# Kernel tuning notes

Measured on AMD Instinct MI355X. Metric: run time of the kernel, lower is better.

The kernel has to match this reference:

```python
import jax, jax.numpy as jnp
import numpy as np

N = 50000          # nodes
E_RAND = 800000    # random edges (avg degree 16)
IN, HID, HEADS, OUT = 256, 64, 4, 40
NEG_SLOPE = 0.2    # PyG GATConv default leaky_relu slope
BN_EPS = 1e-5


def setup_inputs() -> dict:
    key = jax.random.key(0)
    ks = jax.random.split(key, 24)
    x = jax.random.normal(ks[0], (N, IN), jnp.float32)
    ei = jax.random.randint(ks[1], (2, E_RAND), 0, N)
    loops = jnp.arange(N, dtype=ei.dtype)
    edge_index = jnp.concatenate([ei, jnp.stack([loops, loops])], axis=1)  # add self loops (PyG default)
    s = 0.1
    d = {
        "x": x,
        "edge_index": edge_index,
        "W0": jax.random.normal(ks[2], (IN, HEADS * HID), jnp.float32) * s,
        "a_src0": jax.random.normal(ks[3], (HEADS, HID), jnp.float32) * s,
        "a_dst0": jax.random.normal(ks[4], (HEADS, HID), jnp.float32) * s,
        "b0": jax.random.normal(ks[5], (HEADS * HID,), jnp.float32) * s,
        "bn0_g": jnp.ones((HEADS * HID,), jnp.float32),
        "bn0_b": jnp.zeros((HEADS * HID,), jnp.float32),
        "bn0_m": jax.random.normal(ks[6], (HEADS * HID,), jnp.float32) * s,
        "bn0_v": jax.random.uniform(ks[7], (HEADS * HID,), jnp.float32, 0.5, 1.5),
        "W1": jax.random.normal(ks[8], (HEADS * HID, HEADS * HID), jnp.float32) * s,
        "a_src1": jax.random.normal(ks[9], (HEADS, HID), jnp.float32) * s,
        "a_dst1": jax.random.normal(ks[10], (HEADS, HID), jnp.float32) * s,
        "b1": jax.random.normal(ks[11], (HEADS * HID,), jnp.float32) * s,
        "bn1_g": jnp.ones((HEADS * HID,), jnp.float32),
        "bn1_b": jnp.zeros((HEADS * HID,), jnp.float32),
        "bn1_m": jax.random.normal(ks[12], (HEADS * HID,), jnp.float32) * s,
        "bn1_v": jax.random.uniform(ks[13], (HEADS * HID,), jnp.float32, 0.5, 1.5),
        "W2": jax.random.normal(ks[14], (HEADS * HID, OUT), jnp.float32) * s,
        "a_src2": jax.random.normal(ks[15], (1, OUT), jnp.float32) * s,
        "a_dst2": jax.random.normal(ks[16], (1, OUT), jnp.float32) * s,
        "b2": jax.random.normal(ks[17], (OUT,), jnp.float32) * s,
    }
    return d


def gat_conv(x, edge_index, W, att_src, att_dst, heads, ch):
    """PyG GATConv (eval mode): gather -> leaky_relu attn -> segment softmax -> scatter add."""
    src, dst = edge_index[0], edge_index[1]
    h = (x @ W).reshape(-1, heads, ch)                       # [N,H,C]
    a_s = jnp.einsum('nhc,hc->nh', h, att_src)
    a_d = jnp.einsum('nhc,hc->nh', h, att_dst)
    e = jax.nn.leaky_relu(a_s[src] + a_d[dst], NEG_SLOPE)    # [E,H]
    m = jax.ops.segment_max(e, dst, num_segments=N)
    m = jax.lax.stop_gradient(jnp.where(jnp.isfinite(m), m, 0.0))
    p = jnp.exp(e - m[dst])
    denom = jax.ops.segment_sum(p, dst, num_segments=N)
    alpha = p / (denom[dst] + 1e-16)                         # [E,H]
    msg = h[src] * alpha[:, :, None]                         # [E,H,C]
    return jax.ops.segment_sum(msg, dst, num_segments=N)     # [N,H,C]


def _bn(h, g, b, m, v):
    return g * (h - m) * jax.lax.rsqrt(v + BN_EPS) + b


def reference(x, edge_index, W0, a_src0, a_dst0, b0, bn0_g, bn0_b, bn0_m, bn0_v,
              W1, a_src1, a_dst1, b1, bn1_g, bn1_b, bn1_m, bn1_v,
              W2, a_src2, a_dst2, b2):
    h = gat_conv(x, edge_index, W0, a_src0, a_dst0, HEADS, HID).reshape(N, HEADS * HID) + b0
    h = jax.nn.elu(_bn(h, bn0_g, bn0_b, bn0_m, bn0_v))
    h = gat_conv(h, edge_index, W1, a_src1, a_dst1, HEADS, HID).reshape(N, HEADS * HID) + b1
    h = jax.nn.elu(_bn(h, bn1_g, bn1_b, bn1_m, bn1_v))
    out = gat_conv(h, edge_index, W2, a_src2, a_dst2, 1, OUT).reshape(N, OUT) + b2
    return out
```

## Files before the change

### kernel.cpp

```cpp
#include <hip/hip_runtime.h>
#include <cstdint>
#include <cstddef>

constexpr int kN = 50000;
constexpr float kSlope = 0.2f;
constexpr float kBnEps = 1e-5f;

static inline int ceil_div(int a, int b) { return (a + b - 1) / b; }

typedef __attribute__((ext_vector_type(8))) short bf16x8;
typedef __attribute__((ext_vector_type(8))) unsigned short ushortx8;
typedef __attribute__((ext_vector_type(4))) float f32x4;

__device__ inline unsigned short f2bf(float f) {
  unsigned int u = __float_as_uint(f);
  u = (u + 0x7FFFu + ((u >> 16) & 1u)) >> 16;
  return (unsigned short)u;
}
__device__ inline float bf2f(unsigned short h) {
  return __uint_as_float(((unsigned int)h) << 16);
}


__global__ void k_degree(const int* __restrict__ dst, int* __restrict__ deg, int E) {
  int e = blockIdx.x * blockDim.x + threadIdx.x;
  if (e < E) atomicAdd(&deg[dst[e]], 1);
}

__global__ void k_scan1(const int* __restrict__ deg, int* __restrict__ rp,
                        int* __restrict__ bsum, int n) {
  __shared__ int sm[256];
  int i = blockIdx.x * 256 + threadIdx.x;
  int v = (i < n) ? deg[i] : 0;
  sm[threadIdx.x] = v;
  __syncthreads();
  for (int off = 1; off < 256; off <<= 1) {
    int t = (threadIdx.x >= off) ? sm[threadIdx.x - off] : 0;
    __syncthreads();
    sm[threadIdx.x] += t;
    __syncthreads();
  }
  if (i < n) rp[i + 1] = sm[threadIdx.x];
  if (threadIdx.x == 255) bsum[blockIdx.x] = sm[255];
}

__global__ void k_scan2(int* bsum, int nb) {
  __shared__ int sm[256];
  int v = (threadIdx.x < nb) ? bsum[threadIdx.x] : 0;
  sm[threadIdx.x] = v;
  __syncthreads();
  for (int off = 1; off < 256; off <<= 1) {
    int t = (threadIdx.x >= off) ? sm[threadIdx.x - off] : 0;
    __syncthreads();
    sm[threadIdx.x] += t;
    __syncthreads();
  }
  if (threadIdx.x < nb) bsum[threadIdx.x] = sm[threadIdx.x] - v;
}

__global__ void k_scan3(int* __restrict__ rp, const int* __restrict__ bsum, int n) {
  int i = blockIdx.x * 256 + threadIdx.x;
  if (i < n) rp[i + 1] += bsum[blockIdx.x];
  if (i == 0) rp[0] = 0;
}

__global__ void k_scatter(const int* __restrict__ src, const int* __restrict__ dst,
                          const int* __restrict__ rp, int* __restrict__ cur,
                          int* __restrict__ csr, int E) {
  int e = blockIdx.x * blockDim.x + threadIdx.x;
  if (e < E) {
    int d = dst[e];
    int pos = rp[d] + atomicAdd(&cur[d], 1);
    csr[pos] = src[e];
  }
}


__global__ void k_cast(const float* __restrict__ in, unsigned short* __restrict__ out, int n4) {
  int i = blockIdx.x * blockDim.x + threadIdx.x;
  if (i >= n4) return;
  float4 v = ((const float4*)in)[i];
  ushort4 o;
  o.x = f2bf(v.x);
  o.y = f2bf(v.y);
  o.z = f2bf(v.z);
  o.w = f2bf(v.w);
  ((ushort4*)out)[i] = o;
}

__global__ void k_transW3(const float* __restrict__ W0, unsigned short* __restrict__ Wt0,
                          const float* __restrict__ W1, unsigned short* __restrict__ Wt1,
                          const float* __restrict__ W2, unsigned short* __restrict__ Wt2) {
  int i = blockIdx.x * blockDim.x + threadIdx.x;
  const int S0 = 256 * 256, S1 = 256 * 256, S2 = 128 * 256;
  if (i < S0) {
    int nc = i >> 8, k = i & 255;
    Wt0[i] = f2bf(W0[(size_t)k * 256 + nc]);
  } else if (i < S0 + S1) {
    int j = i - S0;
    int nc = j >> 8, k = j & 255;
    Wt1[j] = f2bf(W1[(size_t)k * 256 + nc]);
  } else if (i < S0 + S1 + S2) {
    int j = i - S0 - S1;
    int nc = j >> 8, k = j & 255;
    Wt2[j] = (nc < 40) ? f2bf(W2[(size_t)k * 40 + nc]) : (unsigned short)0;
  }
}


__global__ __launch_bounds__(256) void k_mfma_gemm(
    const unsigned short* __restrict__ A, const unsigned short* __restrict__ Bt,
    unsigned short* __restrict__ C, const float* __restrict__ asrc,
    const float* __restrict__ adst, float* __restrict__ a_s, float* __restrict__ a_d, int M,
    int K, int Nc, int ldc, int heads, int acols) {
  constexpr int BM = 128, BK = 32, LDR = 40;
  __shared__ unsigned short As[BM * LDR];
  __shared__ unsigned short Bs[BM * LDR];
  int tid = threadIdx.x;
  int wave = tid >> 6, lane = tid & 63;
  int quad = lane >> 4, l16 = lane & 15;
  int wm = (wave & 1) * 64, wn = (wave >> 1) * 64;
  int bm = blockIdx.x * BM, bn = blockIdx.y * BM;
  f32x4 acc[4][4] = {};
  for (int k0 = 0; k0 < K; k0 += BK) {
#pragma unroll
    for (int it = 0; it < 2; it++) {
      int c = tid + it * 256;
      int row = c >> 2, part = c & 3;
      int gm = bm + row;
      ushortx8 va = (ushortx8)(0);
      if (gm < M) va = *(const ushortx8*)(A + (size_t)gm * K + k0 + part * 8);
      *(ushortx8*)(As + row * LDR + part * 8) = va;
      ushortx8 vb = *(const ushortx8*)(Bt + (size_t)(bn + row) * K + k0 + part * 8);
      *(ushortx8*)(Bs + row * LDR + part * 8) = vb;
    }
    __syncthreads();
    bf16x8 af[4], bf[4];
#pragma unroll
    for (int i = 0; i < 4; i++) {
      af[i] = *(const bf16x8*)(As + (wm + i * 16 + l16) * LDR + quad * 8);
      bf[i] = *(const bf16x8*)(Bs + (wn + i * 16 + l16) * LDR + quad * 8);
    }
#pragma unroll
    for (int i = 0; i < 4; i++)
#pragma unroll
      for (int j = 0; j < 4; j++)
        acc[i][j] = __builtin_amdgcn_mfma_f32_16x16x32_bf16(af[i], bf[j], acc[i][j], 0, 0, 0);
    __syncthreads();
  }
#pragma unroll
  for (int i = 0; i < 4; i++) {
#pragma unroll
    for (int j = 0; j < 4; j++) {
      int col = bn + wn + j * 16 + l16;
      if (col >= Nc) continue;
#pragma unroll
      for (int r = 0; r < 4; r++) {
        int row = bm + wm + i * 16 + quad * 4 + r;
        if (row < M) C[(size_t)row * ldc + col] = f2bf(acc[i][j][r]);
      }
    }
  }
  int ghead = (bn + wn) >> 6;
  if (ghead < heads) {
    float asv[4], adv[4];
#pragma unroll
    for (int j = 0; j < 4; j++) {
      int col = bn + wn + j * 16 + l16;
      bool ok = col < acols;
      asv[j] = ok ? asrc[col] : 0.f;
      adv[j] = ok ? adst[col] : 0.f;
    }
#pragma unroll
    for (int i = 0; i < 4; i++) {
#pragma unroll
      for (int r = 0; r < 4; r++) {
        float s = acc[i][0][r] * asv[0] + acc[i][1][r] * asv[1] + acc[i][2][r] * asv[2] +
                  acc[i][3][r] * asv[3];
        float d = acc[i][0][r] * adv[0] + acc[i][1][r] * adv[1] + acc[i][2][r] * adv[2] +
                  acc[i][3][r] * adv[3];
#pragma unroll
        for (int mask = 1; mask <= 8; mask <<= 1) {
          s += __shfl_xor(s, mask, 64);
          d += __shfl_xor(d, mask, 64);
        }
        if (l16 == 0) {
          int row = bm + wm + i * 16 + quad * 4 + r;
          if (row < M) {
            a_s[row * heads + ghead] = s;
            a_d[row * heads + ghead] = d;
          }
        }
      }
    }
  }
}


__global__ __launch_bounds__(256) void k_attn_agg256(
    const int* __restrict__ rp, const int* __restrict__ csr, const unsigned short* __restrict__ h,
    const float* __restrict__ a_s, const float* __restrict__ a_d, const float* __restrict__ bias,
    const float* __restrict__ bg, const float* __restrict__ bb, const float* __restrict__ bm,
    const float* __restrict__ bv, unsigned short* __restrict__ out, int n_nodes) {
  int wid = (blockIdx.x * blockDim.x + threadIdx.x) >> 6;
  int n = wid >> 1;
  if (n >= n_nodes) return;
  int chalf = (wid & 1) << 7;
  int lane = threadIdx.x & 63;
  int q = lane >> 4, l16 = lane & 15;
  int c = chalf + l16 * 8;
  int head = c >> 6;
  float ad = a_d[n * 4 + head];
  int beg = rp[n], end = rp[n + 1];
  float acc[8] = {};
  float psum = 0.f;
  int e = beg;
  for (; e + 8 <= end; e += 8) {
    int s0 = csr[e + q];
    int s1 = csr[e + 4 + q];
    float x0 = a_s[s0 * 4 + head] + ad;
    float x1 = a_s[s1 * 4 + head] + ad;
    ushortx8 v0 = *(const ushortx8*)(h + (size_t)s0 * 256 + c);
    ushortx8 v1 = *(const ushortx8*)(h + (size_t)s1 * 256 + c);
    x0 = x0 > 0.f ? x0 : x0 * kSlope;
    x1 = x1 > 0.f ? x1 : x1 * kSlope;
    float p0 = __expf(x0), p1 = __expf(x1);
    psum += p0 + p1;
#pragma unroll
    for (int j = 0; j < 8; j++) acc[j] += bf2f(v0[j]) * p0 + bf2f(v1[j]) * p1;
  }
  int rem = end - e;
  if (q < rem) {
    int s0 = csr[e + q];
    float x0 = a_s[s0 * 4 + head] + ad;
    x0 = x0 > 0.f ? x0 : x0 * kSlope;
    float p0 = __expf(x0);
    psum += p0;
    ushortx8 v0 = *(const ushortx8*)(h + (size_t)s0 * 256 + c);
#pragma unroll
    for (int j = 0; j < 8; j++) acc[j] += bf2f(v0[j]) * p0;
  }
  if (rem > 4 && q < rem - 4) {
    int s1 = csr[e + 4 + q];
    float x1 = a_s[s1 * 4 + head] + ad;
    x1 = x1 > 0.f ? x1 : x1 * kSlope;
    float p1 = __expf(x1);
    psum += p1;
    ushortx8 v1 = *(const ushortx8*)(h + (size_t)s1 * 256 + c);
#pragma unroll
    for (int j = 0; j < 8; j++) acc[j] += bf2f(v1[j]) * p1;
  }
  psum += __shfl_xor(psum, 16, 64);
  psum += __shfl_xor(psum, 32, 64);
#pragma unroll
  for (int j = 0; j < 8; j++) {
    acc[j] += __shfl_xor(acc[j], 16, 64);
    acc[j] += __shfl_xor(acc[j], 32, 64);
  }
  if (q == 0) {
    float rden = 1.f / (psum + 1e-16f);
    ushortx8 o;
#pragma unroll
    for (int j = 0; j < 8; j++) {
      float v = acc[j] * rden + bias[c + j];
      v = bg[c + j] * (v - bm[c + j]) * rsqrtf(bv[c + j] + kBnEps) + bb[c + j];
      v = v > 0.f ? v : (__expf(v) - 1.f);
      o[j] = f2bf(v);
    }
    *(ushortx8*)(out + (size_t)n * 256 + c) = o;
  }
}


__global__ __launch_bounds__(256) void k_attn_agg40(
    const int* __restrict__ rp, const int* __restrict__ csr, const unsigned short* __restrict__ h,
    const float* __restrict__ a_s, const float* __restrict__ a_d, const float* __restrict__ bias,
    float* __restrict__ out, int n_nodes) {
  int wid = (blockIdx.x * blockDim.x + threadIdx.x) >> 6;
  int lane = threadIdx.x & 63;
  if (wid >= n_nodes) return;
  int n = wid;
  int beg = rp[n], end = rp[n + 1];
  float ad = a_d[n];
  int grp = lane >> 3, l8 = lane & 7;
  int c = l8 * 8;
  float acc[8] = {};
  float psum = 0.f;
  for (int base = beg; base < end; base += 16) {
    int e0 = base + grp;
    int e1 = base + 8 + grp;
    if (e0 < end) {
      int s = csr[e0];
      float x = a_s[s] + ad;
      x = x > 0.f ? x : x * kSlope;
      float p = __expf(x);
      psum += p;
      ushortx8 hv = *(const ushortx8*)(h + (size_t)s * 64 + c);
#pragma unroll
      for (int j = 0; j < 8; j++) acc[j] += bf2f(hv[j]) * p;
    }
    if (e1 < end) {
      int s = csr[e1];
      float x = a_s[s] + ad;
      x = x > 0.f ? x : x * kSlope;
      float p = __expf(x);
      psum += p;
      ushortx8 hv = *(const ushortx8*)(h + (size_t)s * 64 + c);
#pragma unroll
      for (int j = 0; j < 8; j++) acc[j] += bf2f(hv[j]) * p;
    }
  }
#pragma unroll
  for (int mask = 8; mask <= 32; mask <<= 1) psum += __shfl_xor(psum, mask, 64);
#pragma unroll
  for (int j = 0; j < 8; j++) {
#pragma unroll
    for (int mask = 8; mask <= 32; mask <<= 1) acc[j] += __shfl_xor(acc[j], mask, 64);
  }
  if (lane < 5) {
    float rden = 1.f / (psum + 1e-16f);
    float4 o0, o1;
    o0.x = acc[0] * rden + bias[c + 0];
    o0.y = acc[1] * rden + bias[c + 1];
    o0.z = acc[2] * rden + bias[c + 2];
    o0.w = acc[3] * rden + bias[c + 3];
    o1.x = acc[4] * rden + bias[c + 4];
    o1.y = acc[5] * rden + bias[c + 5];
    o1.z = acc[6] * rden + bias[c + 6];
    o1.w = acc[7] * rden + bias[c + 7];
    *(float4*)(out + (size_t)n * 40 + c) = o0;
    *(float4*)(out + (size_t)n * 40 + c + 4) = o1;
  }
}


extern "C" void kernel_launch(void* const* d_in, const int* in_sizes, int n_in, void* d_out,
                              int out_size, void* d_ws, size_t ws_size, hipStream_t stream) {
  const float* x = (const float*)d_in[0];
  const int* ei = (const int*)d_in[1];
  const float* W0 = (const float*)d_in[2];
  const float* as0 = (const float*)d_in[3];
  const float* ad0 = (const float*)d_in[4];
  const float* b0 = (const float*)d_in[5];
  const float* bg0 = (const float*)d_in[6];
  const float* bb0 = (const float*)d_in[7];
  const float* bm0 = (const float*)d_in[8];
  const float* bv0 = (const float*)d_in[9];
  const float* W1 = (const float*)d_in[10];
  const float* as1 = (const float*)d_in[11];
  const float* ad1 = (const float*)d_in[12];
  const float* b1 = (const float*)d_in[13];
  const float* bg1 = (const float*)d_in[14];
  const float* bb1 = (const float*)d_in[15];
  const float* bm1 = (const float*)d_in[16];
  const float* bv1 = (const float*)d_in[17];
  const float* W2 = (const float*)d_in[18];
  const float* as2 = (const float*)d_in[19];
  const float* ad2 = (const float*)d_in[20];
  const float* b2 = (const float*)d_in[21];
  float* out = (float*)d_out;

  const int E = in_sizes[1] / 2;
  const int* srcIdx = ei;
  const int* dstIdx = ei + E;

  char* p = (char*)d_ws;
  auto alloc = [&](size_t bytes) -> void* {
    void* r = (void*)p;
    p += (bytes + 255) & ~(size_t)255;
    return r;
  };
  int* rp = (int*)alloc((kN + 1) * sizeof(int));
  int* degcur = (int*)alloc((size_t)2 * kN * sizeof(int));
  int* deg = degcur;
  int* cur = degcur + kN;
  int* bsum = (int*)alloc(256 * sizeof(int));
  int* csr = (int*)alloc((size_t)E * sizeof(int));
  float* a_s = (float*)alloc((size_t)kN * 4 * sizeof(float));
  float* a_d = (float*)alloc((size_t)kN * 4 * sizeof(float));
  unsigned short* x16 = (unsigned short*)alloc((size_t)kN * 256 * 2);
  unsigned short* h16 = (unsigned short*)alloc((size_t)kN * 256 * 2);
  unsigned short* act16 = (unsigned short*)alloc((size_t)kN * 256 * 2);
  unsigned short* Wt0 = (unsigned short*)alloc((size_t)256 * 256 * 2);
  unsigned short* Wt1 = (unsigned short*)alloc((size_t)256 * 256 * 2);
  unsigned short* Wt2 = (unsigned short*)alloc((size_t)128 * 256 * 2);

  const int eb = ceil_div(E, 256);
  const int nb = ceil_div(kN, 256);

  hipMemsetAsync(degcur, 0, (size_t)2 * kN * sizeof(int), stream);
  k_degree<<<eb, 256, 0, stream>>>(dstIdx, deg, E);
  k_scan1<<<nb, 256, 0, stream>>>(deg, rp, bsum, kN);
  k_scan2<<<1, 256, 0, stream>>>(bsum, nb);
  k_scan3<<<nb, 256, 0, stream>>>(rp, bsum, kN);
  k_scatter<<<eb, 256, 0, stream>>>(srcIdx, dstIdx, rp, cur, csr, E);

  k_cast<<<ceil_div(kN * 64, 256), 256, 0, stream>>>(x, x16, kN * 64);
  k_transW3<<<ceil_div(256 * 256 * 2 + 128 * 256, 256), 256, 0, stream>>>(W0, Wt0, W1, Wt1, W2,
                                                                          Wt2);

  dim3 gg(ceil_div(kN, 128), 2);
  dim3 gg2(ceil_div(kN, 128), 1);
  int agg256_blocks = ceil_div(2 * kN, 4);
  int wpn_blocks = ceil_div(kN, 4);

  k_mfma_gemm<<<gg, 256, 0, stream>>>(x16, Wt0, h16, as0, ad0, a_s, a_d, kN, 256, 256, 256, 4,
                                      256);
  k_attn_agg256<<<agg256_blocks, 256, 0, stream>>>(rp, csr, h16, a_s, a_d, b0, bg0, bb0, bm0,
                                                   bv0, act16, kN);

  k_mfma_gemm<<<gg, 256, 0, stream>>>(act16, Wt1, h16, as1, ad1, a_s, a_d, kN, 256, 256, 256, 4,
                                      256);
  k_attn_agg256<<<agg256_blocks, 256, 0, stream>>>(rp, csr, h16, a_s, a_d, b1, bg1, bb1, bm1,
                                                   bv1, act16, kN);

  k_mfma_gemm<<<gg2, 256, 0, stream>>>(act16, Wt2, h16, as2, ad2, a_s, a_d, kN, 256, 40, 64, 1,
                                       40);
  k_attn_agg40<<<wpn_blocks, 256, 0, stream>>>(rp, csr, h16, a_s, a_d, b2, out, kN);
}
```

Before: 479.8 us.

## Switch intermediates to fp16 and use one wave per node in 256-wide aggregation

Replaces the bf16 storage and MFMA with fp16 (f16 MFMA, hardware half conversions) throughout the GEMMs and aggregation kernels. The 256-channel aggregation now assigns one wave per node covering all 256 channels, with each half-wave taking alternate edges and four edges unrolled per iteration. The cross-lane reduction shrinks to a single shuffle stage. The intent is cheaper conversions, fewer reductions, and more loads in flight per lane. It risks fp16 overflow or precision differences and gives lower wave-level parallelism per node.

```diff
diff --git a/kernel.cpp b/kernel.cpp
--- a/kernel.cpp
+++ b/kernel.cpp
@@ -8,17 +8,13 @@
 
 static inline int ceil_div(int a, int b) { return (a + b - 1) / b; }
 
-typedef __attribute__((ext_vector_type(8))) short bf16x8;
+typedef __attribute__((ext_vector_type(8))) _Float16 half8;
 typedef __attribute__((ext_vector_type(8))) unsigned short ushortx8;
 typedef __attribute__((ext_vector_type(4))) float f32x4;
 
-__device__ inline unsigned short f2bf(float f) {
-  unsigned int u = __float_as_uint(f);
-  u = (u + 0x7FFFu + ((u >> 16) & 1u)) >> 16;
-  return (unsigned short)u;
-}
-__device__ inline float bf2f(unsigned short h) {
-  return __uint_as_float(((unsigned int)h) << 16);
+__device__ inline unsigned short f2h_us(float f) {
+  _Float16 h = (_Float16)f;
+  return *(unsigned short*)&h;
 }
 
 
@@ -81,10 +77,10 @@
   if (i >= n4) return;
   float4 v = ((const float4*)in)[i];
   ushort4 o;
-  o.x = f2bf(v.x);
-  o.y = f2bf(v.y);
-  o.z = f2bf(v.z);
-  o.w = f2bf(v.w);
+  o.x = f2h_us(v.x);
+  o.y = f2h_us(v.y);
+  o.z = f2h_us(v.z);
+  o.w = f2h_us(v.w);
   ((ushort4*)out)[i] = o;
 }
 
@@ -95,15 +91,15 @@
   const int S0 = 256 * 256, S1 = 256 * 256, S2 = 128 * 256;
   if (i < S0) {
     int nc = i >> 8, k = i & 255;
-    Wt0[i] = f2bf(W0[(size_t)k * 256 + nc]);
+    Wt0[i] = f2h_us(W0[(size_t)k * 256 + nc]);
   } else if (i < S0 + S1) {
     int j = i - S0;
     int nc = j >> 8, k = j & 255;
-    Wt1[j] = f2bf(W1[(size_t)k * 256 + nc]);
+    Wt1[j] = f2h_us(W1[(size_t)k * 256 + nc]);
   } else if (i < S0 + S1 + S2) {
     int j = i - S0 - S1;
     int nc = j >> 8, k = j & 255;
-    Wt2[j] = (nc < 40) ? f2bf(W2[(size_t)k * 40 + nc]) : (unsigned short)0;
+    Wt2[j] = (nc < 40) ? f2h_us(W2[(size_t)k * 40 + nc]) : (unsigned short)0;
   }
 }
 
@@ -135,17 +131,17 @@
       *(ushortx8*)(Bs + row * LDR + part * 8) = vb;
     }
     __syncthreads();
-    bf16x8 af[4], bf[4];
+    half8 af[4], bf[4];
 #pragma unroll
     for (int i = 0; i < 4; i++) {
-      af[i] = *(const bf16x8*)(As + (wm + i * 16 + l16) * LDR + quad * 8);
-      bf[i] = *(const bf16x8*)(Bs + (wn + i * 16 + l16) * LDR + quad * 8);
+      af[i] = *(const half8*)(As + (wm + i * 16 + l16) * LDR + quad * 8);
+      bf[i] = *(const half8*)(Bs + (wn + i * 16 + l16) * LDR + quad * 8);
     }
 #pragma unroll
     for (int i = 0; i < 4; i++)
 #pragma unroll
       for (int j = 0; j < 4; j++)
-        acc[i][j] = __builtin_amdgcn_mfma_f32_16x16x32_bf16(af[i], bf[j], acc[i][j], 0, 0, 0);
+        acc[i][j] = __builtin_amdgcn_mfma_f32_16x16x32_f16(af[i], bf[j], acc[i][j], 0, 0, 0);
     __syncthreads();
   }
 #pragma unroll
@@ -157,7 +153,7 @@
 #pragma unroll
       for (int r = 0; r < 4; r++) {
         int row = bm + wm + i * 16 + quad * 4 + r;
-        if (row < M) C[(size_t)row * ldc + col] = f2bf(acc[i][j][r]);
+        if (row < M) C[(size_t)row * ldc + col] = f2h_us(acc[i][j][r]);
       }
     }
   }
@@ -198,66 +194,72 @@
 
 
 __global__ __launch_bounds__(256) void k_attn_agg256(
-    const int* __restrict__ rp, const int* __restrict__ csr, const unsigned short* __restrict__ h,
+    const int* __restrict__ rp, const int* __restrict__ csr, const _Float16* __restrict__ h,
     const float* __restrict__ a_s, const float* __restrict__ a_d, const float* __restrict__ bias,
     const float* __restrict__ bg, const float* __restrict__ bb, const float* __restrict__ bm,
     const float* __restrict__ bv, unsigned short* __restrict__ out, int n_nodes) {
   int wid = (blockIdx.x * blockDim.x + threadIdx.x) >> 6;
-  int n = wid >> 1;
-  if (n >= n_nodes) return;
-  int chalf = (wid & 1) << 7;
   int lane = threadIdx.x & 63;
-  int q = lane >> 4, l16 = lane & 15;
-  int c = chalf + l16 * 8;
-  int head = c >> 6;
+  if (wid >= n_nodes) return;
+  int n = wid;
+  int beg = rp[n], end = rp[n + 1];
+  int half = lane >> 5, l32 = lane & 31;
+  int head = l32 >> 3;
+  int c = l32 * 8;
   float ad = a_d[n * 4 + head];
-  int beg = rp[n], end = rp[n + 1];
   float acc[8] = {};
   float psum = 0.f;
   int e = beg;
   for (; e + 8 <= end; e += 8) {
-    int s0 = csr[e + q];
-    int s1 = csr[e + 4 + q];
+    int s0 = csr[e + half];
+    int s1 = csr[e + 2 + half];
+    int s2 = csr[e + 4 + half];
+    int s3 = csr[e + 6 + half];
     float x0 = a_s[s0 * 4 + head] + ad;
     float x1 = a_s[s1 * 4 + head] + ad;
-    ushortx8 v0 = *(const ushortx8*)(h + (size_t)s0 * 256 + c);
-    ushortx8 v1 = *(const ushortx8*)(h + (size_t)s1 * 256 + c);
+    float x2 = a_s[s2 * 4 + head] + ad;
+    float x3 = a_s[s3 * 4 + head] + ad;
+    half8 v0 = *(const half8*)(h + (size_t)s0 * 256 + c);
+    half8 v1 = *(const half8*)(h + (size_t)s1 * 256 + c);
+    half8 v2 = *(const half8*)(h + (size_t)s2 * 256 + c);
+    half8 v3 = *(const half8*)(h + (size_t)s3 * 256 + c);
     x0 = x0 > 0.f ? x0 : x0 * kSlope;
     x1 = x1 > 0.f ? x1 : x1 * kSlope;
+    x2 = x2 > 0.f ? x2 : x2 * kSlope;
+    x3 = x3 > 0.f ? x3 : x3 * kSlope;
     float p0 = __expf(x0), p1 = __expf(x1);
-    psum += p0 + p1;
-#pragma unroll
-    for (int j = 0; j < 8; j++) acc[j] += bf2f(v0[j]) * p0 + bf2f(v1[j]) * p1;
-  }
-  int rem = end - e;
-  if (q < rem) {
-    int s0 = csr[e + q];
+    float p2 = __expf(x2), p3 = __expf(x3);
+    psum += (p0 + p1) + (p2 + p3);
+#pragma unroll
+    for (int j = 0; j < 8; j++) {
+      acc[j] += (float)v0[j] * p0 + (float)v1[j] * p1;
+      acc[j] += (float)v2[j] * p2 + (float)v3[j] * p3;
+    }
+  }
+  for (; e + 2 <= end; e += 2) {
+    int s0 = csr[e + half];
     float x0 = a_s[s0 * 4 + head] + ad;
     x0 = x0 > 0.f ? x0 : x0 * kSlope;
     float p0 = __expf(x0);
     psum += p0;
-    ushortx8 v0 = *(const ushortx8*)(h + (size_t)s0 * 256 + c);
-#pragma unroll
-    for (int j = 0; j < 8; j++) acc[j] += bf2f(v0[j]) * p0;
-  }
-  if (rem > 4 && q < rem - 4) {
-    int s1 = csr[e + 4 + q];
-    float x1 = a_s[s1 * 4 + head] + ad;
-    x1 = x1 > 0.f ? x1 : x1 * kSlope;
-    float p1 = __expf(x1);
-    psum += p1;
-    ushortx8 v1 = *(const ushortx8*)(h + (size_t)s1 * 256 + c);
-#pragma unroll
-    for (int j = 0; j < 8; j++) acc[j] += bf2f(v1[j]) * p1;
-  }
-  psum += __shfl_xor(psum, 16, 64);
+    half8 v0 = *(const half8*)(h + (size_t)s0 * 256 + c);
+#pragma unroll
+    for (int j = 0; j < 8; j++) acc[j] += (float)v0[j] * p0;
+  }
+  if (e < end && half == 0) {
+    int s0 = csr[e];
+    float x0 = a_s[s0 * 4 + head] + ad;
+    x0 = x0 > 0.f ? x0 : x0 * kSlope;
+    float p0 = __expf(x0);
+    psum += p0;
+    half8 v0 = *(const half8*)(h + (size_t)s0 * 256 + c);
+#pragma unroll
+    for (int j = 0; j < 8; j++) acc[j] += (float)v0[j] * p0;
+  }
   psum += __shfl_xor(psum, 32, 64);
 #pragma unroll
-  for (int j = 0; j < 8; j++) {
-    acc[j] += __shfl_xor(acc[j], 16, 64);
-    acc[j] += __shfl_xor(acc[j], 32, 64);
-  }
-  if (q == 0) {
+  for (int j = 0; j < 8; j++) acc[j] += __shfl_xor(acc[j], 32, 64);
+  if (half == 0) {
     float rden = 1.f / (psum + 1e-16f);
     ushortx8 o;
 #pragma unroll
@@ -265,7 +267,7 @@
       float v = acc[j] * rden + bias[c + j];
       v = bg[c + j] * (v - bm[c + j]) * rsqrtf(bv[c + j] + kBnEps) + bb[c + j];
       v = v > 0.f ? v : (__expf(v) - 1.f);
-      o[j] = f2bf(v);
+      o[j] = f2h_us(v);
     }
     *(ushortx8*)(out + (size_t)n * 256 + c) = o;
   }
@@ -273,7 +275,7 @@
 
 
 __global__ __launch_bounds__(256) void k_attn_agg40(
-    const int* __restrict__ rp, const int* __restrict__ csr, const unsigned short* __restrict__ h,
+    const int* __restrict__ rp, const int* __restrict__ csr, const _Float16* __restrict__ h,
     const float* __restrict__ a_s, const float* __restrict__ a_d, const float* __restrict__ bias,
     float* __restrict__ out, int n_nodes) {
   int wid = (blockIdx.x * blockDim.x + threadIdx.x) >> 6;
@@ -295,9 +297,9 @@
       x = x > 0.f ? x : x * kSlope;
       float p = __expf(x);
       psum += p;
-      ushortx8 hv = *(const ushortx8*)(h + (size_t)s * 64 + c);
-#pragma unroll
-      for (int j = 0; j < 8; j++) acc[j] += bf2f(hv[j]) * p;
+      half8 hv = *(const half8*)(h + (size_t)s * 64 + c);
+#pragma unroll
+      for (int j = 0; j < 8; j++) acc[j] += (float)hv[j] * p;
     }
     if (e1 < end) {
       int s = csr[e1];
@@ -305,9 +307,9 @@
       x = x > 0.f ? x : x * kSlope;
       float p = __expf(x);
       psum += p;
-      ushortx8 hv = *(const ushortx8*)(h + (size_t)s * 64 + c);
-#pragma unroll
-      for (int j = 0; j < 8; j++) acc[j] += bf2f(hv[j]) * p;
+      half8 hv = *(const half8*)(h + (size_t)s * 64 + c);
+#pragma unroll
+      for (int j = 0; j < 8; j++) acc[j] += (float)hv[j] * p;
     }
   }
 #pragma unroll
@@ -401,20 +403,20 @@
 
   dim3 gg(ceil_div(kN, 128), 2);
   dim3 gg2(ceil_div(kN, 128), 1);
-  int agg256_blocks = ceil_div(2 * kN, 4);
   int wpn_blocks = ceil_div(kN, 4);
 
   k_mfma_gemm<<<gg, 256, 0, stream>>>(x16, Wt0, h16, as0, ad0, a_s, a_d, kN, 256, 256, 256, 4,
                                       256);
-  k_attn_agg256<<<agg256_blocks, 256, 0, stream>>>(rp, csr, h16, a_s, a_d, b0, bg0, bb0, bm0,
-                                                   bv0, act16, kN);
+  k_attn_agg256<<<wpn_blocks, 256, 0, stream>>>(rp, csr, (const _Float16*)h16, a_s, a_d, b0, bg0,
+                                                bb0, bm0, bv0, act16, kN);
 
   k_mfma_gemm<<<gg, 256, 0, stream>>>(act16, Wt1, h16, as1, ad1, a_s, a_d, kN, 256, 256, 256, 4,
                                       256);
-  k_attn_agg256<<<agg256_blocks, 256, 0, stream>>>(rp, csr, h16, a_s, a_d, b1, bg1, bb1, bm1,
-                                                   bv1, act16, kN);
+  k_attn_agg256<<<wpn_blocks, 256, 0, stream>>>(rp, csr, (const _Float16*)h16, a_s, a_d, b1, bg1,
+                                                bb1, bm1, bv1, act16, kN);
 
   k_mfma_gemm<<<gg2, 256, 0, stream>>>(act16, Wt2, h16, as2, ad2, a_s, a_d, kN, 256, 40, 64, 1,
                                        40);
-  k_attn_agg40<<<wpn_blocks, 256, 0, stream>>>(rp, csr, h16, a_s, a_d, b2, out, kN);
-}
+  k_attn_agg40<<<wpn_blocks, 256, 0, stream>>>(rp, csr, (const _Float16*)h16, a_s, a_d, b2, out,
+                                               kN);
+}
```

Result: faster. 455.7 us (-5.0%).
